# Optimization experiments

Measured on AMD Instinct MI355X. Metric: run time of the kernel, lower is better.

Reference implementation:

```python
import jax, jax.numpy as jnp
import numpy as np

S_DIM = 1024      # sequence_state_dim
INNER = 32        # inner_dim
PAIR = 128        # pairwise_state_dim
EPS = 1e-5


def setup_inputs() -> dict:
    key = jax.random.key(0)
    ks = jax.random.split(key, 6)
    B, L = 1, 1024
    sequence_state = jax.random.normal(ks[0], (B, L, S_DIM), dtype=jnp.float32)
    # LayerNorm params
    ln_gamma = jnp.ones((S_DIM,), dtype=jnp.float32)
    ln_beta = jnp.zeros((S_DIM,), dtype=jnp.float32)
    # proj: Linear(S_DIM -> 2*INNER), bias initialized to zeros in the module
    proj_w = jax.random.normal(ks[1], (S_DIM, 2 * INNER), dtype=jnp.float32) / np.sqrt(S_DIM)
    proj_b = jnp.zeros((2 * INNER,), dtype=jnp.float32)
    # o_proj: Linear(2*INNER -> PAIR), bias zeros
    o_w = jax.random.normal(ks[2], (2 * INNER, PAIR), dtype=jnp.float32) / np.sqrt(2 * INNER)
    o_b = jnp.zeros((PAIR,), dtype=jnp.float32)
    return {
        "sequence_state": sequence_state,
        "ln_gamma": ln_gamma,
        "ln_beta": ln_beta,
        "proj_w": proj_w,
        "proj_b": proj_b,
        "o_w": o_w,
        "o_b": o_b,
    }


def reference(sequence_state, ln_gamma, ln_beta, proj_w, proj_b, o_w, o_b):
    # LayerNorm over last dim
    mu = jnp.mean(sequence_state, axis=-1, keepdims=True)
    var = jnp.mean(jnp.square(sequence_state - mu), axis=-1, keepdims=True)
    s = (sequence_state - mu) * jax.lax.rsqrt(var + EPS) * ln_gamma + ln_beta
    # proj to q, k  [B, L, INNER] each
    s = jnp.einsum("bld,dh->blh", s, proj_w) + proj_b
    q, k = s[..., :INNER], s[..., INNER:]
    # pair features: prod[b,i,j,c] = q[b,j,c]*k[b,i,c]; diff = q[b,j,c]-k[b,i,c]
    prod = q[:, None, :, :] * k[:, :, None, :]   # [B, L, L, INNER]
    diff = q[:, None, :, :] - k[:, :, None, :]   # [B, L, L, INNER]
    x = jnp.concatenate([prod, diff], axis=-1)   # [B, L, L, 2*INNER]
    return jnp.einsum("bijc,cp->bijp", x, o_w) + o_b  # [B, L, L, PAIR]
```

## Files before the change

kernel.cpp:

```cpp
#include <hip/hip_runtime.h>
#include <hip/hip_bf16.h>

#define S_DIM 1024
#define INNER 32
#define PAIR  128
#define LSEQ  1024

typedef float f2 __attribute__((ext_vector_type(2)));

__global__ __launch_bounds__(256) void ln_proj_kernel(
    const float* __restrict__ x,
    const float* __restrict__ gamma,
    const float* __restrict__ beta,
    const float* __restrict__ pw,
    const float* __restrict__ pb,
    const float* __restrict__ ow,
    float* __restrict__ qk,
    float* __restrict__ Aq,
    float* __restrict__ Ak)
{
    const int row  = blockIdx.x;
    const int t    = threadIdx.x;
    const int lane = t & 63;
    const int wv   = t >> 6;

    __shared__ float s_sh[S_DIM];
    __shared__ float wsum[4], wsum2[4];
    __shared__ float hpart[4][64];
    __shared__ float h_sh[64];

    float4 xv = ((const float4*)(x + (size_t)row * S_DIM))[t];
    float sum = xv.x + xv.y + xv.z + xv.w;
    float sq  = xv.x*xv.x + xv.y*xv.y + xv.z*xv.z + xv.w*xv.w;
    #pragma unroll
    for (int off = 32; off; off >>= 1) {
        sum += __shfl_down(sum, off, 64);
        sq  += __shfl_down(sq,  off, 64);
    }
    if (lane == 0) { wsum[wv] = sum; wsum2[wv] = sq; }
    __syncthreads();
    float tot  = wsum[0] + wsum[1] + wsum[2] + wsum[3];
    float tot2 = wsum2[0] + wsum2[1] + wsum2[2] + wsum2[3];
    float mu   = tot * (1.0f / S_DIM);
    float var  = tot2 * (1.0f / S_DIM) - mu * mu;
    float rstd = rsqrtf(var + 1e-5f);

    float4 gv = ((const float4*)gamma)[t];
    float4 bv = ((const float4*)beta)[t];
    float4 sv;
    sv.x = (xv.x - mu) * rstd * gv.x + bv.x;
    sv.y = (xv.y - mu) * rstd * gv.y + bv.y;
    sv.z = (xv.z - mu) * rstd * gv.z + bv.z;
    sv.w = (xv.w - mu) * rstd * gv.w + bv.w;
    ((float4*)s_sh)[t] = sv;
    __syncthreads();

    {
        const int c    = lane;
        const int part = wv;
        const int dbase = part * 256;
        const float* pwp = pw + c;
        float acc = 0.f;
        #pragma unroll 8
        for (int d = 0; d < 256; ++d) {
            acc = fmaf(s_sh[dbase + d], pwp[(size_t)(dbase + d) * 64], acc);
        }
        hpart[part][c] = acc;
    }
    __syncthreads();
    if (t < 64) {
        float h = hpart[0][t] + hpart[1][t] + hpart[2][t] + hpart[3][t] + pb[t];
        h_sh[t] = h;
        qk[(size_t)row * 64 + t] = h;
    }
    __syncthreads();

    {
        const int p    = t & 127;
        const int half = t >> 7;
        const float* w2 = ow + 32 * PAIR + p;
        const float* hh = h_sh + half * 32;
        float acc = 0.f;
        #pragma unroll
        for (int c = 0; c < 32; ++c)
            acc = fmaf(hh[c], w2[(size_t)c * PAIR], acc);
        if (half == 0) Aq[(size_t)row * PAIR + p] = acc;
        else           Ak[(size_t)row * PAIR + p] = acc;
    }
}

__global__ __launch_bounds__(256) void pair_kernel(
    const float* __restrict__ qk,
    const float* __restrict__ Aq,
    const float* __restrict__ Ak,
    const float* __restrict__ ow,
    const float* __restrict__ ob,
    float* __restrict__ out)
{
    const int i    = blockIdx.x;
    const int jblk = blockIdx.y;
    const int lane = threadIdx.x & 63;
    const int wv   = threadIdx.x >> 6;

    f2 kw[32];
    {
        const float4* k4 = (const float4*)(qk + (size_t)i * 64 + 32);
        #pragma unroll
        for (int c4 = 0; c4 < 8; ++c4) {
            float4 kv = k4[c4];
            const f2* w1a = (const f2*)(ow + (size_t)(c4*4+0) * PAIR);
            const f2* w1b = (const f2*)(ow + (size_t)(c4*4+1) * PAIR);
            const f2* w1c = (const f2*)(ow + (size_t)(c4*4+2) * PAIR);
            const f2* w1d = (const f2*)(ow + (size_t)(c4*4+3) * PAIR);
            kw[c4*4+0] = kv.x * w1a[lane];
            kw[c4*4+1] = kv.y * w1b[lane];
            kw[c4*4+2] = kv.z * w1c[lane];
            kw[c4*4+3] = kv.w * w1d[lane];
        }
    }

    const f2 bias = ((const f2*)ob)[lane] - ((const f2*)(Ak + (size_t)i * PAIR))[lane];
    const f2* Aq2 = (const f2*)Aq;
    f2* out2 = (f2*)out;

    const int jbase = jblk * 128 + wv * 32;
    #pragma unroll 2
    for (int jj = 0; jj < 32; jj += 2) {
        const int j0 = __builtin_amdgcn_readfirstlane(jbase + jj);
        const int j1 = j0 + 1;
        const float4* q40 = (const float4*)(qk + (size_t)j0 * 64);
        const float4* q41 = (const float4*)(qk + (size_t)j1 * 64);

        f2 a0 = bias + Aq2[(size_t)j0 * 64 + lane];
        f2 a1 = bias + Aq2[(size_t)j1 * 64 + lane];
        f2 b0 = {0.f, 0.f};
        f2 b1 = {0.f, 0.f};

        #pragma unroll
        for (int c4 = 0; c4 < 4; ++c4) {
            float4 qv0 = q40[c4];
            float4 qv1 = q41[c4];
            a0 += qv0.x * kw[c4*4+0];  a1 += qv1.x * kw[c4*4+0];
            a0 += qv0.y * kw[c4*4+1];  a1 += qv1.y * kw[c4*4+1];
            a0 += qv0.z * kw[c4*4+2];  a1 += qv1.z * kw[c4*4+2];
            a0 += qv0.w * kw[c4*4+3];  a1 += qv1.w * kw[c4*4+3];
        }
        #pragma unroll
        for (int c4 = 4; c4 < 8; ++c4) {
            float4 qv0 = q40[c4];
            float4 qv1 = q41[c4];
            b0 += qv0.x * kw[c4*4+0];  b1 += qv1.x * kw[c4*4+0];
            b0 += qv0.y * kw[c4*4+1];  b1 += qv1.y * kw[c4*4+1];
            b0 += qv0.z * kw[c4*4+2];  b1 += qv1.z * kw[c4*4+2];
            b0 += qv0.w * kw[c4*4+3];  b1 += qv1.w * kw[c4*4+3];
        }
        a0 += b0;
        a1 += b1;

        const size_t off0 = ((size_t)i * LSEQ + (size_t)j0) * (PAIR / 2);
        __builtin_nontemporal_store(a0, out2 + off0 + lane);
        __builtin_nontemporal_store(a1, out2 + off0 + 64 + lane);
    }
}

extern "C" void kernel_launch(void* const* d_in, const int* in_sizes, int n_in,
                              void* d_out, int out_size, void* d_ws, size_t ws_size,
                              hipStream_t stream) {
    const float* x     = (const float*)d_in[0];
    const float* gamma = (const float*)d_in[1];
    const float* beta  = (const float*)d_in[2];
    const float* pw    = (const float*)d_in[3];
    const float* pb    = (const float*)d_in[4];
    const float* ow    = (const float*)d_in[5];
    const float* ob    = (const float*)d_in[6];
    float* out = (float*)d_out;

    float* qk = (float*)d_ws;
    float* Aq = qk + (size_t)LSEQ * 64;
    float* Ak = Aq + (size_t)LSEQ * PAIR;

    ln_proj_kernel<<<dim3(LSEQ), dim3(256), 0, stream>>>(
        x, gamma, beta, pw, pb, ow, qk, Aq, Ak);

    pair_kernel<<<dim3(LSEQ, 8), dim3(256), 0, stream>>>(
        qk, Aq, Ak, ow, ob, out);
}
```

Measured before the change: 569.7 us.

## Double-buffer q-row prefetch in pair kernel and raise occupancy hint

Restructures the pair kernel's j loop so the q rows and Aq entries for the next pair of output rows are loaded into register buffers while the current row's FMAs and stores run. This is meant to hide load latency behind compute and the output stores. It also adds a min-blocks-per-CU hint of 4 to launch_bounds, which caps per-thread registers. That cap may cause spills given the 32-entry kw array plus two 8-float4 buffers. The last iteration prefetches two rows past the block's range, reading into the adjacent workspace; this is harmless but unused.

```diff
diff --git a/kernel.cpp b/kernel.cpp
--- a/kernel.cpp
+++ b/kernel.cpp
@@ -89,7 +89,7 @@
     }
 }
 
-__global__ __launch_bounds__(256) void pair_kernel(
+__global__ __launch_bounds__(256, 4) void pair_kernel(
     const float* __restrict__ qk,
     const float* __restrict__ Aq,
     const float* __restrict__ Ak,
@@ -124,43 +124,56 @@
     f2* out2 = (f2*)out;
 
     const int jbase = jblk * 128 + wv * 32;
-    #pragma unroll 2
+    const int j0    = __builtin_amdgcn_readfirstlane(jbase);
+    f2* op = out2 + ((size_t)i * LSEQ + (size_t)j0) * (PAIR / 2) + lane;
+
+    #define LDQ(buf, row) {                                                  \
+        const float4* _s = (const float4*)(qk + (size_t)(row) * 64);         \
+        _Pragma("unroll")                                                    \
+        for (int _c = 0; _c < 8; ++_c) buf[_c] = _s[_c];                     \
+    }
+
+    float4 qa[8], qb[8];
+    f2 aqa, aqb;
+    LDQ(qa, j0);     aqa = Aq2[(size_t)j0 * 64 + lane];
+    LDQ(qb, j0 + 1); aqb = Aq2[(size_t)(j0 + 1) * 64 + lane];
+
+    #pragma unroll 1
     for (int jj = 0; jj < 32; jj += 2) {
-        const int j0 = __builtin_amdgcn_readfirstlane(jbase + jj);
-        const int j1 = j0 + 1;
-        const float4* q40 = (const float4*)(qk + (size_t)j0 * 64);
-        const float4* q41 = (const float4*)(qk + (size_t)j1 * 64);
-
-        f2 a0 = bias + Aq2[(size_t)j0 * 64 + lane];
-        f2 a1 = bias + Aq2[(size_t)j1 * 64 + lane];
-        f2 b0 = {0.f, 0.f};
-        f2 b1 = {0.f, 0.f};
-
-        #pragma unroll
-        for (int c4 = 0; c4 < 4; ++c4) {
-            float4 qv0 = q40[c4];
-            float4 qv1 = q41[c4];
-            a0 += qv0.x * kw[c4*4+0];  a1 += qv1.x * kw[c4*4+0];
-            a0 += qv0.y * kw[c4*4+1];  a1 += qv1.y * kw[c4*4+1];
-            a0 += qv0.z * kw[c4*4+2];  a1 += qv1.z * kw[c4*4+2];
-            a0 += qv0.w * kw[c4*4+3];  a1 += qv1.w * kw[c4*4+3];
-        }
-        #pragma unroll
-        for (int c4 = 4; c4 < 8; ++c4) {
-            float4 qv0 = q40[c4];
-            float4 qv1 = q41[c4];
-            b0 += qv0.x * kw[c4*4+0];  b1 += qv1.x * kw[c4*4+0];
-            b0 += qv0.y * kw[c4*4+1];  b1 += qv1.y * kw[c4*4+1];
-            b0 += qv0.z * kw[c4*4+2];  b1 += qv1.z * kw[c4*4+2];
-            b0 += qv0.w * kw[c4*4+3];  b1 += qv1.w * kw[c4*4+3];
-        }
-        a0 += b0;
-        a1 += b1;
-
-        const size_t off0 = ((size_t)i * LSEQ + (size_t)j0) * (PAIR / 2);
-        __builtin_nontemporal_store(a0, out2 + off0 + lane);
-        __builtin_nontemporal_store(a1, out2 + off0 + 64 + lane);
-    }
+        {
+            f2 a = {0.f, 0.f}, b = {0.f, 0.f};
+            #pragma unroll
+            for (int c4 = 0; c4 < 4; ++c4) {
+                float4 q0 = qa[c4];
+                float4 q1 = qa[c4 + 4];
+                a += q0.x * kw[c4*4+0];   b += q1.x * kw[16 + c4*4+0];
+                a += q0.y * kw[c4*4+1];   b += q1.y * kw[16 + c4*4+1];
+                a += q0.z * kw[c4*4+2];   b += q1.z * kw[16 + c4*4+2];
+                a += q0.w * kw[c4*4+3];   b += q1.w * kw[16 + c4*4+3];
+            }
+            f2 r = (a + b) + (bias + aqa);
+            __builtin_nontemporal_store(r, op + (size_t)jj * (PAIR / 2));
+            LDQ(qa, j0 + jj + 2);
+            aqa = Aq2[(size_t)(j0 + jj + 2) * 64 + lane];
+        }
+        {
+            f2 a = {0.f, 0.f}, b = {0.f, 0.f};
+            #pragma unroll
+            for (int c4 = 0; c4 < 4; ++c4) {
+                float4 q0 = qb[c4];
+                float4 q1 = qb[c4 + 4];
+                a += q0.x * kw[c4*4+0];   b += q1.x * kw[16 + c4*4+0];
+                a += q0.y * kw[c4*4+1];   b += q1.y * kw[16 + c4*4+1];
+                a += q0.z * kw[c4*4+2];   b += q1.z * kw[16 + c4*4+2];
+                a += q0.w * kw[c4*4+3];   b += q1.w * kw[16 + c4*4+3];
+            }
+            f2 r = (a + b) + (bias + aqb);
+            __builtin_nontemporal_store(r, op + (size_t)(jj + 1) * (PAIR / 2));
+            LDQ(qb, j0 + jj + 3);
+            aqb = Aq2[(size_t)(j0 + jj + 3) * 64 + lane];
+        }
+    }
+    #undef LDQ
 }
 
 extern "C" void kernel_launch(void* const* d_in, const int* in_sizes, int n_in,
```

After: 566.8 us. No clear change (-0.5%).
